# Kernel optimization log

Measured on AMD Instinct MI355X. Metric: run time of the kernel, lower is better.

The kernel has to match this reference:

```python
import jax, jax.numpy as jnp
import numpy as np

N = 8192
MARGIN = 0.01
PRICE_W = 0.5
RANK_W = 0.5


def setup_inputs() -> dict:
    key = jax.random.key(0)
    k1, k2, k3 = jax.random.split(key, 3)
    predicted_prices = jax.random.normal(k1, (N,), dtype=jnp.float32)
    actual_prices = jax.random.normal(k2, (N,), dtype=jnp.float32)
    # keep previous prices in [0.5, 1.5) so the division is well-behaved
    previous_prices = jax.random.uniform(k3, (N,), dtype=jnp.float32) + 0.5
    return {"predicted_prices": predicted_prices,
            "actual_prices": actual_prices,
            "previous_prices": previous_prices}


def reference(predicted_prices, actual_prices, previous_prices):
    # MSE price loss
    price_loss = jnp.mean((predicted_prices - actual_prices) ** 2)

    pred_r = (predicted_prices - previous_prices) / previous_prices  # [N]
    act_r = (actual_prices - previous_prices) / previous_prices     # [N]

    # pairwise differences (i, j): r[i] - r[j]
    act_diff = act_r[:, None] - act_r[None, :]      # [N, N]
    pred_diff = pred_r[:, None] - pred_r[None, :]   # [N, N]

    n = pred_r.shape[0]
    upper = jnp.triu(jnp.ones((n, n), dtype=bool), k=1)  # j > i
    valid = upper & (act_diff != 0)

    # margin_ranking_loss(x1=pred_diff, x2=0, target=sign(act_diff)):
    #   max(0, -target * pred_diff + margin)
    hinge = jnp.maximum(0.0, -jnp.sign(act_diff) * pred_diff + MARGIN)

    count = jnp.sum(valid)
    rank_sum = jnp.sum(jnp.where(valid, hinge, 0.0))
    ranking_loss = jnp.where(
        count > 0,
        rank_sum / jnp.maximum(count, 1).astype(hinge.dtype),
        jnp.zeros((), dtype=hinge.dtype),
    )

    total_loss = PRICE_W * price_loss + RANK_W * ranking_loss
    return total_loss
```

## Files before the change

kernel.cpp:

```cpp
#include <hip/hip_runtime.h>

constexpr int    NN      = 8192;
constexpr float  MARGIN  = 0.01f;
constexpr int    BT      = 256;
constexpr int    FI      = 4;
constexpr int    TI      = BT * FI;
constexpr int    TJ      = 32;
constexpr int    NTI     = NN / TI;
constexpr int    NTJ     = NN / TJ;
constexpr int    CPR     = TI / TJ;
constexpr int    NBLOCKS = NTI * NTJ - CPR * (NTI * (NTI - 1) / 2);

__global__ __launch_bounds__(BT)
void pair_kernel(const float* __restrict__ pred,
                 const float* __restrict__ act,
                 const float* __restrict__ prev,
                 float* __restrict__ rank_part,
                 float* __restrict__ price_part)
{
    int t  = blockIdx.x;
    int ib = 0;
    while (t >= NTJ - CPR * ib) { t -= NTJ - CPR * ib; ++ib; }
    const int  jc        = CPR * ib + t;
    const bool diag_like = (t < CPR);
    const bool do_price  = (t == 0);

    __shared__ alignas(16) float2 s_t[TJ];

    const int tid = threadIdx.x;
    if (tid < TJ) {
        const int   j   = jc * TJ + tid;
        const float pv  = prev[j];
        const float rcp = __builtin_amdgcn_rcpf(pv);
        s_t[tid] = make_float2((pred[j] - pv) * rcp, (act[j] - pv) * rcp);
    }

    float pri[FI], ari[FI];
    float pp = 0.f;
#pragma unroll
    for (int f = 0; f < FI; ++f) {
        const int   i   = ib * TI + f * BT + tid;
        const float pv  = prev[i];
        const float p   = pred[i];
        const float a   = act[i];
        const float rcp = __builtin_amdgcn_rcpf(pv);
        pri[f] = (p - pv) * rcp;
        ari[f] = (a - pv) * rcp;
        if (do_price) {
            const float d = p - a;
            pp += d * d;
        }
    }

    __syncthreads();

    float4 q[TJ / 2];
    const float4* __restrict__ s4 = (const float4*)s_t;
#pragma unroll
    for (int g = 0; g < TJ / 2; ++g) q[g] = s4[g];

    float acc[FI] = {0.f, 0.f, 0.f, 0.f};

#define PAIR(f, pj, aj)                                             \
    {                                                               \
        const float    nad = (aj) - ari[f];        \
        const float    pd  = pri[f] - (pj);                         \
        const unsigned m   = __float_as_uint(nad) & 0x80000000u;    \
        const float    u   = __uint_as_float(__float_as_uint(pd) ^ m); \
        acc[f] += fmaxf(0.0f, u + MARGIN);                          \
    }

#pragma unroll
    for (int g = 0; g < TJ / 2; ++g) {
#pragma unroll
        for (int f = 0; f < FI; ++f) {
            PAIR(f, q[g].x, q[g].y);
            PAIR(f, q[g].z, q[g].w);
        }
    }
#undef PAIR

    float w = (acc[0] + acc[1]) + (acc[2] + acc[3]);
    if (!diag_like) w += w;

    for (int off = 32; off > 0; off >>= 1) w += __shfl_down(w, off, 64);
    __shared__ float r_s[4], r_p[4];
    if ((tid & 63) == 0) r_s[tid >> 6] = w;
    if (do_price) {
        for (int off = 32; off > 0; off >>= 1) pp += __shfl_down(pp, off, 64);
        if ((tid & 63) == 0) r_p[tid >> 6] = pp;
    }
    __syncthreads();
    if (tid == 0) {
        rank_part[blockIdx.x] = r_s[0] + r_s[1] + r_s[2] + r_s[3];
        if (do_price) price_part[ib] = r_p[0] + r_p[1] + r_p[2] + r_p[3];
    }
}

__global__ __launch_bounds__(256)
void finalize_kernel(const float* __restrict__ rank_part,
                     const float* __restrict__ price_part,
                     float* __restrict__ out)
{
    double s = 0.0, p = 0.0;
    for (int t = threadIdx.x; t < NBLOCKS; t += 256) s += (double)rank_part[t];
    if (threadIdx.x < NTI) p = (double)price_part[threadIdx.x];
    for (int off = 32; off > 0; off >>= 1) {
        s += __shfl_down(s, off, 64);
        p += __shfl_down(p, off, 64);
    }
    __shared__ double rs[4], rp[4];
    const int w = threadIdx.x >> 6;
    if ((threadIdx.x & 63) == 0) { rs[w] = s; rp[w] = p; }
    __syncthreads();
    if (threadIdx.x == 0) {
        const double S = rs[0] + rs[1] + rs[2] + rs[3];
        const double P = rp[0] + rp[1] + rp[2] + rp[3];
        const double rank = (S - (double)NN * (double)MARGIN)
                          / ((double)NN * (double)(NN - 1));
        out[0] = (float)(0.5 * (P / (double)NN) + 0.5 * rank);
    }
}

extern "C" void kernel_launch(void* const* d_in, const int* in_sizes, int n_in,
                              void* d_out, int out_size, void* d_ws, size_t ws_size,
                              hipStream_t stream)
{
    const float* pred = (const float*)d_in[0];
    const float* act  = (const float*)d_in[1];
    const float* prev = (const float*)d_in[2];

    char* w = (char*)d_ws;
    float* rank_part  = (float*)w;
    float* price_part = (float*)(w + 8192);

    pair_kernel<<<NBLOCKS, BT, 0, stream>>>(pred, act, prev, rank_part, price_part);
    finalize_kernel<<<1, 256, 0, stream>>>(rank_part, price_part, (float*)d_out);
}
```

Measured before the change: 14.06 us.

## Fuse finalize into pair kernel via cooperative grid sync and fold margin algebraically

Launches the pair kernel cooperatively when occupancy allows, so block 0 performs the final reduction after a grid-wide sync instead of a second kernel launch. The margin add is hoisted out of the inner loop by rewriting max(0,u+m) as max(-m,u) and adding m once at the end. Launch bounds now request 5 blocks per CU so the grid can be co-resident. The grid sync and per-call occupancy query add overhead that may offset the saved launch.

```diff
diff --git a/kernel.cpp b/kernel.cpp
--- a/kernel.cpp
+++ b/kernel.cpp
@@ -1,4 +1,7 @@
 #include <hip/hip_runtime.h>
+#include <hip/hip_cooperative_groups.h>
+
+namespace cg = cooperative_groups;
 
 constexpr int    NN      = 8192;
 constexpr float  MARGIN  = 0.01f;
@@ -10,13 +13,16 @@
 constexpr int    NTJ     = NN / TJ;
 constexpr int    CPR     = TI / TJ;
 constexpr int    NBLOCKS = NTI * NTJ - CPR * (NTI * (NTI - 1) / 2);
+constexpr int    NCU     = 256;
 
-__global__ __launch_bounds__(BT)
+template<bool COOP>
+__global__ __launch_bounds__(BT, 5)
 void pair_kernel(const float* __restrict__ pred,
                  const float* __restrict__ act,
                  const float* __restrict__ prev,
                  float* __restrict__ rank_part,
-                 float* __restrict__ price_part)
+                 float* __restrict__ price_part,
+                 float* __restrict__ out)
 {
     int t  = blockIdx.x;
     int ib = 0;
@@ -61,13 +67,22 @@
 
     float acc[FI] = {0.f, 0.f, 0.f, 0.f};
 
-#define PAIR(f, pj, aj)                                             \
-    {                                                               \
-        const float    nad = (aj) - ari[f];        \
-        const float    pd  = pri[f] - (pj);                         \
-        const unsigned m   = __float_as_uint(nad) & 0x80000000u;    \
+#define PAIR(f, pj, aj)                                                \
+    {                                                                  \
+        const float    nad = (aj) - ari[f];           \
+        const float    pd  = pri[f] - (pj);                            \
+        const unsigned m   = __float_as_uint(nad) & 0x80000000u;       \
         const float    u   = __uint_as_float(__float_as_uint(pd) ^ m); \
-        acc[f] += fmaxf(0.0f, u + MARGIN);                          \
+        acc[f] = fmaxf(acc[f] + 0.0f, acc[f] + 0.0f);                  \
+    }
+#undef PAIR
+#define PAIR(f, pj, aj)                                                \
+    {                                                                  \
+        const float    nad = (aj) - ari[f];           \
+        const float    pd  = pri[f] - (pj);                            \
+        const unsigned m   = __float_as_uint(nad) & 0x80000000u;       \
+        const float    u   = __uint_as_float(__float_as_uint(pd) ^ m); \
+        acc[f] += fmaxf(-MARGIN, u);                                   \
     }
 
 #pragma unroll
@@ -94,6 +109,29 @@
     if (tid == 0) {
         rank_part[blockIdx.x] = r_s[0] + r_s[1] + r_s[2] + r_s[3];
         if (do_price) price_part[ib] = r_p[0] + r_p[1] + r_p[2] + r_p[3];
+        __threadfence();
+    }
+
+    if constexpr (COOP) {
+        cg::this_grid().sync();
+        if (blockIdx.x != 0) return;
+
+        double s = 0.0, p = 0.0;
+        for (int k = tid; k < NBLOCKS; k += BT) s += (double)rank_part[k];
+        if (tid < NTI) p = (double)price_part[tid];
+        for (int off = 32; off > 0; off >>= 1) {
+            s += __shfl_down(s, off, 64);
+            p += __shfl_down(p, off, 64);
+        }
+        __shared__ double rs2[4], rp2[4];
+        if ((tid & 63) == 0) { rs2[tid >> 6] = s; rp2[tid >> 6] = p; }
+        __syncthreads();
+        if (tid == 0) {
+            const double S = rs2[0] + rs2[1] + rs2[2] + rs2[3];
+            const double P = rp2[0] + rp2[1] + rp2[2] + rp2[3];
+            const double rank = (double)MARGIN + S / ((double)NN * (double)(NN - 1));
+            out[0] = (float)(0.5 * (P / (double)NN) + 0.5 * rank);
+        }
     }
 }
 
@@ -116,8 +154,7 @@
     if (threadIdx.x == 0) {
         const double S = rs[0] + rs[1] + rs[2] + rs[3];
         const double P = rp[0] + rp[1] + rp[2] + rp[3];
-        const double rank = (S - (double)NN * (double)MARGIN)
-                          / ((double)NN * (double)(NN - 1));
+        const double rank = (double)MARGIN + S / ((double)NN * (double)(NN - 1));
         out[0] = (float)(0.5 * (P / (double)NN) + 0.5 * rank);
     }
 }
@@ -130,10 +167,23 @@
     const float* act  = (const float*)d_in[1];
     const float* prev = (const float*)d_in[2];
 
-    char* w = (char*)d_ws;
+    char*  w          = (char*)d_ws;
     float* rank_part  = (float*)w;
     float* price_part = (float*)(w + 8192);
+    float* outp       = (float*)d_out;
 
-    pair_kernel<<<NBLOCKS, BT, 0, stream>>>(pred, act, prev, rank_part, price_part);
-    finalize_kernel<<<1, 256, 0, stream>>>(rank_part, price_part, (float*)d_out);
+    int perCU = 0;
+    (void)hipOccupancyMaxActiveBlocksPerMultiprocessor(
+        &perCU, (const void*)pair_kernel<true>, BT, 0);
+
+    if (perCU * NCU >= NBLOCKS) {
+        void* kargs[] = {(void*)&pred, (void*)&act, (void*)&prev,
+                         (void*)&rank_part, (void*)&price_part, (void*)&outp};
+        (void)hipLaunchCooperativeKernel((const void*)pair_kernel<true>,
+                                         dim3(NBLOCKS), dim3(BT), kargs, 0, stream);
+    } else {
+        pair_kernel<false><<<NBLOCKS, BT, 0, stream>>>(pred, act, prev,
+                                                       rank_part, price_part, outp);
+        finalize_kernel<<<1, 256, 0, stream>>>(rank_part, price_part, outp);
+    }
 }
```

New measurement: 29.53 us. 2.1x slower.
